# Performance work log

Measured on AMD Instinct MI355X. Metric: run time of the kernel, lower is better.

## Reference

```python
import jax, jax.numpy as jnp
import numpy as np

B, T, D, N, K, H = 2, 2048, 2048, 16, 8, 128
WINDOW = 1024
SOFT_CAP = 50.0
Q_SCALE = H ** -0.5  # query_pre_attn_scalar
ROPE_BASE = 10000
ROPE_SCALE = 1.0
K_MASK = -2.3819763e38


def apply_rope(x, positions, base_frequency=ROPE_BASE, scale_factor=ROPE_SCALE):
    # x: [B, T, n, H], positions: [B, T]
    head_dim = x.shape[-1]
    fraction = 2.0 * jnp.arange(head_dim // 2, dtype=jnp.float32) / head_dim
    timescale = base_frequency ** fraction  # [H/2]
    sin_inp = positions[..., None].astype(jnp.float32) / timescale  # [B,T,H/2]
    sin_inp = sin_inp[..., None, :] / scale_factor  # [B,T,1,H/2]
    sin, cos = jnp.sin(sin_inp), jnp.cos(sin_inp)
    x1, x2 = jnp.split(x, 2, axis=-1)
    out = jnp.concatenate([x1 * cos - x2 * sin, x2 * cos + x1 * sin], axis=-1)
    return out.astype(x.dtype)


def rms_norm(x, scale, eps=1e-6):
    var = jnp.mean(jnp.square(x.astype(jnp.float32)), axis=-1, keepdims=True)
    normed = x * jax.lax.rsqrt(var + eps)
    return (normed * (1.0 + scale)).astype(x.dtype)


def setup_inputs() -> dict:
    key = jax.random.key(0)
    ks = jax.random.split(key, 4)
    x = jax.random.normal(ks[0], (B, T, D), jnp.float32)
    segment_pos = jnp.tile(jnp.arange(T, dtype=jnp.int32)[None, :], (B, 1))
    attn_mask = jnp.tril(jnp.ones((T, T), dtype=bool))[None].repeat(B, axis=0)
    w_q = jax.random.normal(ks[1], (N, D, H), jnp.float32) * (D ** -0.5)
    w_kv = jax.random.normal(ks[2], (2, K, D, H), jnp.float32) * (D ** -0.5)
    w_o = jax.random.normal(ks[3], (N, H, D), jnp.float32) * ((N * H) ** -0.5)
    q_norm_scale = jnp.zeros((H,), jnp.float32)
    k_norm_scale = jnp.zeros((H,), jnp.float32)
    return dict(x=x, w_q=w_q, w_kv=w_kv, w_o=w_o,
                q_norm_scale=q_norm_scale, k_norm_scale=k_norm_scale,
                segment_pos=segment_pos, attn_mask=attn_mask)


def reference(x, w_q, w_kv, w_o, q_norm_scale, k_norm_scale, segment_pos, attn_mask):
    # projections
    q = jnp.einsum('BTD,NDH->BTNH', x, w_q)              # [B,T,N,H]
    kv = jnp.einsum('BSD,CKDH->CBSKH', x, w_kv)          # [2,B,S,K,H]
    k, v = kv[0], kv[1]
    # QK RMSNorm
    q = rms_norm(q, q_norm_scale)
    k = rms_norm(k, k_norm_scale)
    # RoPE + query scaling
    q = apply_rope(q, segment_pos) * Q_SCALE
    k = apply_rope(k, segment_pos)
    # GQA logits
    G = N // K
    qg = q.reshape(B, T, K, G, H)
    logits = jnp.einsum('BTKGH,BSKH->BTKGS', qg, k).reshape(B, T, N, T)
    # soft cap
    logits = jnp.tanh(logits / SOFT_CAP) * SOFT_CAP
    # sliding-window mask combined with causal attn_mask
    pos_q = segment_pos[:, :, None]
    pos_k = segment_pos[:, None, :]
    sliding = (pos_k > pos_q - WINDOW) & (pos_k < pos_q + WINDOW)
    mask = attn_mask & sliding                           # [B,T,S]
    padded = jnp.where(mask[:, :, None, :], logits, K_MASK)
    probs = jax.nn.softmax(padded, axis=-1).astype(k.dtype)
    # GQA weighted values
    enc = jnp.einsum('BTKGS,BSKH->BTKGH', probs.reshape(B, T, K, G, T), v)
    enc = enc.reshape(B, T, N, H)
    # split/concat of navigator vs scribe heads is an identity on output
    return jnp.einsum('BTNH,NHD->BTD', enc, w_o)
```

## Files before the change

kernel.cpp:

```cpp
#include <hip/hip_runtime.h>
#include <hip/hip_bf16.h>
#include <stdint.h>

typedef __attribute__((ext_vector_type(8))) short short8;
typedef __attribute__((ext_vector_type(4))) float f32x4;

#define B_ 2
#define T_ 2048
#define D_ 2048
#define N_ 16
#define KH_ 8
#define H_ 128
#define WINDOW_ 1024

__device__ __forceinline__ uint16_t f2bf(float f) {
  union { float f; uint32_t u; } a; a.f = f;
  uint32_t u = a.u;
  return (uint16_t)((u + 0x7FFFu + ((u >> 16) & 1u)) >> 16);
}
__device__ __forceinline__ float bf2f(uint16_t u) {
  union { uint32_t u; float f; } a; a.u = (uint32_t)u << 16;
  return a.f;
}

__device__ __forceinline__ void gl_lds16(const void* g, void* l) {
  __builtin_amdgcn_global_load_lds((const __attribute__((address_space(1))) void*)g,
                                   (__attribute__((address_space(3))) void*)l, 16, 0, 0);
}

__global__ __launch_bounds__(256) void k_f2b4(const float* __restrict__ src,
                                              uint16_t* __restrict__ dst, long n) {
  long i = ((long)blockIdx.x * 256 + threadIdx.x) * 4;
  if (i >= n) return;
  float4 v = *(const float4*)(src + i);
  uint64_t p = (uint64_t)f2bf(v.x) | ((uint64_t)f2bf(v.y) << 16) |
               ((uint64_t)f2bf(v.z) << 32) | ((uint64_t)f2bf(v.w) << 48);
  *(uint64_t*)(dst + i) = p;
}

__global__ __launch_bounds__(256)
void k_prep_qkv(const float* __restrict__ w_q, const float* __restrict__ w_kv,
                uint16_t* __restrict__ wq_t, uint16_t* __restrict__ wkv_t) {
  __shared__ float tile[32][33];
  int z = blockIdx.z;
  const float* s;
  uint16_t* d;
  if (z < 16) {
    s = w_q + (long)z * D_ * H_;
    d = wq_t + (long)z * H_ * D_;
  } else if (z < 24) {
    s = w_kv + (long)(z - 16) * D_ * H_;
    d = wkv_t + (long)(z - 16) * H_ * D_;
  } else {
    s = w_kv + (long)KH_ * D_ * H_ + (long)(z - 24) * D_ * H_;
    d = wkv_t + (long)1024 * 2048 + (long)(z - 24) * H_ * D_;
  }
  int c0 = blockIdx.x * 32, r0 = blockIdx.y * 32;
  int x = threadIdx.x, y = threadIdx.y;
#pragma unroll
  for (int j = 0; j < 4; ++j)
    tile[y + j * 8][x] = s[(long)(r0 + y + j * 8) * H_ + (c0 + x)];
  __syncthreads();
#pragma unroll
  for (int j = 0; j < 4; ++j)
    d[(long)(c0 + y + j * 8) * D_ + (r0 + x)] = f2bf(tile[x][y + j * 8]);
}

__global__ __launch_bounds__(256)
void k_transpose_f2b(const float* __restrict__ src, uint16_t* __restrict__ dst,
                     int R, int C, int nb1, long sbs1, long sbs2, long dbs,
                     long src_off, int srs) {
  __shared__ float tile[32][33];
  int z = blockIdx.z;
  int b1 = z % nb1, b2 = z / nb1;
  const float* s = src + src_off + (long)b1 * sbs1 + (long)b2 * sbs2;
  uint16_t* d = dst + (long)z * dbs;
  int c0 = blockIdx.x * 32, r0 = blockIdx.y * 32;
  int x = threadIdx.x, y = threadIdx.y;
#pragma unroll
  for (int j = 0; j < 4; ++j)
    tile[y + j * 8][x] = s[(long)(r0 + y + j * 8) * srs + (c0 + x)];
  __syncthreads();
#pragma unroll
  for (int j = 0; j < 4; ++j)
    d[(long)(c0 + y + j * 8) * R + (r0 + x)] = f2bf(tile[x][y + j * 8]);
}

__global__ __launch_bounds__(256)
void k_transpose_v(const uint16_t* __restrict__ kvg, uint16_t* __restrict__ vbt) {
  __shared__ uint16_t tile[32][33];
  int z = blockIdx.z;
  int kh = z % KH_, b = z / KH_;
  const uint16_t* s = kvg + (long)b * T_ * 2048 + 1024 + kh * H_;
  uint16_t* d = vbt + (long)z * H_ * T_;
  int h0 = blockIdx.x * 32, s0 = blockIdx.y * 32;
  int x = threadIdx.x, y = threadIdx.y;
#pragma unroll
  for (int j = 0; j < 4; ++j)
    tile[y + j * 8][x] = s[(long)(s0 + y + j * 8) * 2048 + (h0 + x)];
  __syncthreads();
#pragma unroll
  for (int j = 0; j < 4; ++j) {
    int h = h0 + y + j * 8;
    int si = s0 + x;
    int ss = (si & ~63) | ((((si >> 3) & 7) ^ (h & 7)) << 3) | (si & 7);
    d[(long)h * T_ + ss] = tile[x][y + j * 8];
  }
}

__global__ __launch_bounds__(512, 2)
void k_gemm8(const uint16_t* __restrict__ A, const uint16_t* __restrict__ Bt,
             uint16_t* __restrict__ C0, uint16_t* __restrict__ C1, int nbx, int splitc) {
  __shared__ __align__(16) uint16_t Ls[2][2][2][128 * 64];
  int tid = threadIdx.x, lane = tid & 63, w = tid >> 6;
  int wm = w >> 2, wn = w & 3;
  int fr = lane & 15, fgrp = lane >> 4;
  int bid = blockIdx.x;
  int k2 = bid >> 3;
  long by = (bid & 7) * 2 + k2 / nbx;
  long bx = k2 % nbx;
  long row0 = by * 256, col0 = bx * 256;

  int trow = tid >> 3;
  int kse = (((tid & 7) * 16) ^ ((trow & 7) << 4)) >> 1;
  const uint16_t* aS[2] = { A + (row0 + trow) * 2048 + kse,
                            A + (row0 + 128 + trow) * 2048 + kse };
  const uint16_t* bS[2] = { Bt + (col0 + trow) * 2048 + kse,
                            Bt + (col0 + 128 + trow) * 2048 + kse };
  char* ldsbase = (char*)Ls + w * 1024;

  int kx[2] = { (fgrp * 16) ^ ((fr & 7) << 4), (64 + fgrp * 16) ^ ((fr & 7) << 4) };
  int aoffb = (wm * 64 + fr) * 128;
  int boffb = (wn * 32 + fr) * 128;
  const char* LA = (const char*)Ls;
  const char* LB = LA + 65536;

  f32x4 acc[2][2][4][2];
#pragma unroll
  for (int qm = 0; qm < 2; ++qm)
#pragma unroll
    for (int qn = 0; qn < 2; ++qn)
#pragma unroll
      for (int m = 0; m < 4; ++m)
#pragma unroll
        for (int n = 0; n < 2; ++n) acc[qm][qn][m][n] = (f32x4){0.f, 0.f, 0.f, 0.f};

  short8 RA[4][2];
  short8 RB[2][2][2];

#define STG(MAT, SLOT, HALF, KT) do {                                      \
    const uint16_t* _g = (MAT ? bS[HALF] : aS[HALF]) + (KT) * 64;          \
    char* _l = ldsbase + (MAT) * 65536 + (SLOT) * 32768 + (HALF) * 16384;  \
    gl_lds16(_g, _l);                                                      \
    gl_lds16(_g + 64 * 2048, _l + 8192);                                   \
  } while (0)

#define RDA(SLOT, QM) do {                                                             \
    _Pragma("unroll") for (int m = 0; m < 4; ++m) {                                    \
      RA[m][0] = *(const short8*)(LA + (SLOT)*32768 + (QM)*16384 + aoffb + m*2048 + kx[0]); \
      RA[m][1] = *(const short8*)(LA + (SLOT)*32768 + (QM)*16384 + aoffb + m*2048 + kx[1]); } \
  } while (0)

#define RDB(SLOT, QN) do {                                                             \
    _Pragma("unroll") for (int n = 0; n < 2; ++n) {                                    \
      RB[QN][n][0] = *(const short8*)(LB + (SLOT)*32768 + (QN)*16384 + boffb + n*2048 + kx[0]); \
      RB[QN][n][1] = *(const short8*)(LB + (SLOT)*32768 + (QN)*16384 + boffb + n*2048 + kx[1]); } \
  } while (0)

#define PHX(RDSTMT, STGSTMT, QM, QN, VM) do {                                         \
    RDSTMT;                                                                           \
    STGSTMT;                                                                          \
    __builtin_amdgcn_s_barrier();                                                     \
    asm volatile("s_waitcnt lgkmcnt(0)" ::: "memory");                                \
    __builtin_amdgcn_sched_barrier(0);                                                \
    __builtin_amdgcn_s_setprio(1);                                                    \
    _Pragma("unroll") for (int m = 0; m < 4; ++m)                                     \
      _Pragma("unroll") for (int n = 0; n < 2; ++n) {                                 \
        acc[QM][QN][m][n] = __builtin_amdgcn_mfma_f32_16x16x32_bf16(RA[m][0], RB[QN][n][0], acc[QM][QN][m][n], 0, 0, 0); \
        acc[QM][QN][m][n] = __builtin_amdgcn_mfma_f32_16x16x32_bf16(RA[m][1], RB[QN][n][1], acc[QM][QN][m][n], 0, 0, 0); } \
    __builtin_amdgcn_s_setprio(0);                                                    \
    if (VM) { asm volatile("s_waitcnt vmcnt(8)" ::: "memory");                        \
              __builtin_amdgcn_sched_barrier(0); }                                    \
    __builtin_amdgcn_s_barrier();                                                     \
    __builtin_amdgcn_sched_barrier(0);                                                \
  } while (0)

  STG(0, 0, 0, 0); STG(1, 0, 0, 0); STG(1, 0, 1, 0); STG(0, 0, 1, 0);
  STG(0, 1, 0, 1); STG(1, 1, 0, 1); STG(1, 1, 1, 1); STG(0, 1, 1, 1);
  asm volatile("s_waitcnt vmcnt(8)" ::: "memory");
  __builtin_amdgcn_sched_barrier(0);
  __builtin_amdgcn_s_barrier();

#pragma unroll 1
  for (int it = 0; it < 16; ++it) {
    int t2 = (2 * it + 2) & 31, t3 = (2 * it + 3) & 31;
    PHX({ RDA(0, 0); RDB(0, 0); }, {}, 0, 0, 0);
    PHX({ RDB(0, 1); }, { STG(0, 0, 0, t2); STG(1, 0, 0, t2); }, 0, 1, 0);
    PHX({ RDA(0, 1); }, { STG(1, 0, 1, t2); }, 1, 1, 0);
    PHX({}, { STG(0, 0, 1, t2); }, 1, 0, 1);
    PHX({ RDA(1, 0); RDB(1, 0); }, {}, 0, 0, 0);
    PHX({ RDB(1, 1); }, { STG(0, 1, 0, t3); STG(1, 1, 0, t3); }, 0, 1, 0);
    PHX({ RDA(1, 1); }, { STG(1, 1, 1, t3); }, 1, 1, 0);
    PHX({}, { STG(0, 1, 1, t3); }, 1, 0, 1);
  }
#undef PHX
#undef RDA
#undef RDB
#undef STG

  int og = fgrp * 4;
  bool hic = (col0 >= splitc);
  uint16_t* Cb = hic ? C1 : C0;
  long cb = col0 - (hic ? splitc : 0);
#pragma unroll
  for (int qm = 0; qm < 2; ++qm)
#pragma unroll
    for (int qn = 0; qn < 2; ++qn)
#pragma unroll
      for (int m = 0; m < 4; ++m)
#pragma unroll
        for (int n = 0; n < 2; ++n) {
          long r = row0 + qm * 128 + wm * 64 + m * 16 + og;
          long c = cb + qn * 128 + wn * 32 + n * 16 + fr;
          uint16_t* cp = Cb + r * 2048 + c;
#pragma unroll
          for (int i = 0; i < 4; ++i) cp[(long)i * 2048] = f2bf(acc[qm][qn][m][n][i]);
        }
}

__global__ __launch_bounds__(512, 2)
void k_gemm8n(const uint16_t* __restrict__ A, const uint16_t* __restrict__ Bt,
              float* __restrict__ C, int nbx) {
  __shared__ __align__(16) uint16_t LsA[2][2][128 * 64];
  __shared__ __align__(16) uint16_t LsB[2][128 * 64];
  int tid = threadIdx.x, lane = tid & 63, w = tid >> 6;
  int wm = w >> 2, wn = w & 3;
  int fr = lane & 15, fgrp = lane >> 4;
  int bid = blockIdx.x;
  int k2 = bid >> 3;
  long by = (bid & 7) * 2 + k2 / nbx;
  long bx = k2 % nbx;
  long row0 = by * 256, col0 = bx * 128;

  int trow = tid >> 3;
  int kse = (((tid & 7) * 16) ^ ((trow & 7) << 4)) >> 1;
  const uint16_t* aS[2] = { A + (row0 + trow) * 2048 + kse,
                            A + (row0 + 128 + trow) * 2048 + kse };
  const uint16_t* bS = Bt + (col0 + trow) * 2048 + kse;
  char* ldsA_w = (char*)LsA + w * 1024;
  char* ldsB_w = (char*)LsB + w * 1024;

  int kx[2] = { (fgrp * 16) ^ ((fr & 7) << 4), (64 + fgrp * 16) ^ ((fr & 7) << 4) };
  int aoffb = (wm * 64 + fr) * 128;
  int boffb = (wn * 32 + fr) * 128;
  const char* LA = (const char*)LsA;
  const char* LB = (const char*)LsB;

  f32x4 acc[2][4][2];
#pragma unroll
  for (int qm = 0; qm < 2; ++qm)
#pragma unroll
    for (int m = 0; m < 4; ++m)
#pragma unroll
      for (int n = 0; n < 2; ++n) acc[qm][m][n] = (f32x4){0.f, 0.f, 0.f, 0.f};

#define STGA(SLOT, HALF, KT) do {                                \
    const uint16_t* _g = aS[HALF] + (KT) * 64;                   \
    char* _l = ldsA_w + (SLOT) * 32768 + (HALF) * 16384;         \
    gl_lds16(_g, _l);                                            \
    gl_lds16(_g + 64 * 2048, _l + 8192);                         \
  } while (0)
#define STGB(SLOT, KT) do {                                      \
    const uint16_t* _g = bS + (KT) * 64;                         \
    char* _l = ldsB_w + (SLOT) * 16384;                          \
    gl_lds16(_g, _l);                                            \
    gl_lds16(_g + 64 * 2048, _l + 8192);                         \
  } while (0)

#define PHN(SLOT, QM, STMT, VM) do {                                                  \
    short8 _a[4][2], _b[2][2];                                                        \
    _Pragma("unroll") for (int m = 0; m < 4; ++m) {                                   \
      _a[m][0] = *(const short8*)(LA + (SLOT)*32768 + (QM)*16384 + aoffb + m*2048 + kx[0]); \
      _a[m][1] = *(const short8*)(LA + (SLOT)*32768 + (QM)*16384 + aoffb + m*2048 + kx[1]); } \
    _Pragma("unroll") for (int n = 0; n < 2; ++n) {                                   \
      _b[n][0] = *(const short8*)(LB + (SLOT)*16384 + boffb + n*2048 + kx[0]);        \
      _b[n][1] = *(const short8*)(LB + (SLOT)*16384 + boffb + n*2048 + kx[1]); }      \
    STMT;                                                                             \
    __builtin_amdgcn_s_barrier();                                                     \
    asm volatile("s_waitcnt lgkmcnt(0)" ::: "memory");                                \
    __builtin_amdgcn_sched_barrier(0);                                                \
    __builtin_amdgcn_s_setprio(1);                                                    \
    _Pragma("unroll") for (int m = 0; m < 4; ++m)                                     \
      _Pragma("unroll") for (int n = 0; n < 2; ++n) {                                 \
        acc[QM][m][n] = __builtin_amdgcn_mfma_f32_16x16x32_bf16(_a[m][0], _b[n][0], acc[QM][m][n], 0, 0, 0); \
        acc[QM][m][n] = __builtin_amdgcn_mfma_f32_16x16x32_bf16(_a[m][1], _b[n][1], acc[QM][m][n], 0, 0, 0); } \
    __builtin_amdgcn_s_setprio(0);                                                    \
    if (VM) { asm volatile("s_waitcnt vmcnt(2)" ::: "memory");                        \
              __builtin_amdgcn_sched_barrier(0); }                                    \
    __builtin_amdgcn_s_barrier();                                                     \
    __builtin_amdgcn_sched_barrier(0);                                                \
  } while (0)

  STGA(0, 0, 0); STGA(0, 1, 0); STGB(0, 0); STGA(1, 0, 1);
  asm volatile("s_waitcnt vmcnt(2)" ::: "memory");
  __builtin_amdgcn_sched_barrier(0);
  __builtin_amdgcn_s_barrier();

#pragma unroll 1
  for (int it = 0; it < 16; ++it) {
    int t1 = 2 * it + 1, t2 = (2 * it + 2) & 31, t3 = (2 * it + 3) & 31;
    PHN(0, 0, { STGA(1, 1, t1); STGB(1, t1); }, 0);
    PHN(0, 1, STGA(0, 0, t2), 1);
    PHN(1, 0, { STGA(0, 1, t2); STGB(0, t2); }, 0);
    PHN(1, 1, STGA(1, 0, t3), 1);
  }
#undef PHN
#undef STGA
#undef STGB

  int og = fgrp * 4;
#pragma unroll
  for (int qm = 0; qm < 2; ++qm)
#pragma unroll
    for (int m = 0; m < 4; ++m)
#pragma unroll
      for (int n = 0; n < 2; ++n) {
        long r = row0 + qm * 128 + wm * 64 + m * 16 + og;
        long c = col0 + wn * 32 + n * 16 + fr;
        float* cp = C + r * 2048 + c;
#pragma unroll
        for (int i = 0; i < 4; ++i) cp[(long)i * 2048] = acc[qm][m][n][i];
      }
}

__global__ __launch_bounds__(256)
void k_qpost(const uint16_t* __restrict__ qg, const float* __restrict__ qs,
             uint16_t* __restrict__ qb) {
  int gw = blockIdx.x * 4 + (threadIdx.x >> 6);
  int lane = threadIdx.x & 63;
  int bt = gw / N_;
  int t = bt % T_;
  const uint16_t* src = qg + (long)gw * H_;
  float x1 = bf2f(src[lane]), x2 = bf2f(src[lane + 64]);
  float ssq = x1 * x1 + x2 * x2;
#pragma unroll
  for (int off = 1; off < 64; off <<= 1) ssq += __shfl_xor(ssq, off);
  float inv = rsqrtf(ssq * (1.0f / 128.0f) + 1e-6f);
  float n1 = x1 * inv * (1.0f + qs[lane]);
  float n2 = x2 * inv * (1.0f + qs[lane + 64]);
  float ts = powf(10000.0f, (float)lane * (2.0f / 128.0f));
  float ang = (float)t / ts;
  float sn, cs;
  sincosf(ang, &sn, &cs);
  const float QSC = 0.08838834764831845f;
  uint16_t* dp = qb + (long)gw * H_;
  dp[lane] = f2bf((n1 * cs - n2 * sn) * QSC);
  dp[lane + 64] = f2bf((n2 * cs + n1 * sn) * QSC);
}

__global__ __launch_bounds__(256)
void k_kpost(const uint16_t* __restrict__ kvg, const float* __restrict__ ks,
             uint16_t* __restrict__ kb) {
  int gw = blockIdx.x * 4 + (threadIdx.x >> 6);
  int lane = threadIdx.x & 63;
  int kh = gw % KH_;
  int bt = gw / KH_;
  int t = bt % T_, b = bt / T_;
  const uint16_t* src = kvg + (long)bt * (KH_ * H_ * 2) + kh * H_;
  float x1 = bf2f(src[lane]), x2 = bf2f(src[lane + 64]);
  float ssq = x1 * x1 + x2 * x2;
#pragma unroll
  for (int off = 1; off < 64; off <<= 1) ssq += __shfl_xor(ssq, off);
  float inv = rsqrtf(ssq * (1.0f / 128.0f) + 1e-6f);
  float n1 = x1 * inv * (1.0f + ks[lane]);
  float n2 = x2 * inv * (1.0f + ks[lane + 64]);
  float ts = powf(10000.0f, (float)lane * (2.0f / 128.0f));
  float ang = (float)t / ts;
  float sn, cs;
  sincosf(ang, &sn, &cs);
  int sw = (t & 7) << 3;
  uint16_t* dp = kb + ((long)(b * KH_ + kh) * T_ + t) * H_;
  dp[lane ^ sw] = f2bf(n1 * cs - n2 * sn);
  dp[(lane + 64) ^ sw] = f2bf(n2 * cs + n1 * sn);
}

__global__ __launch_bounds__(256, 2)
void k_attn(const uint16_t* __restrict__ qb, const uint16_t* __restrict__ kb,
            const uint16_t* __restrict__ vbt, uint16_t* __restrict__ enc) {
  __shared__ uint16_t Ks[2][64 * 128];
  __shared__ uint16_t Vs[2][128 * 64];
  __shared__ uint16_t Pl[4][16 * 64];
  int tid = threadIdx.x, lane = tid & 63, w = tid >> 6;
  int nt = T_ / 64;
  int blk = blockIdx.x;
  int tq = nt - 1 - (blk >> 5);
  int bn = blk & 31;
  int n = bn % N_, b = bn / N_;
  int kh = n >> 1;
  int t0 = tq * 64;
  int tw = t0 + w * 16;
  int fr = lane & 15, fgrp = lane >> 4, fk = fgrp * 8;
  int sw3 = fr & 7;

  const uint16_t* qrow = qb + ((long)(b * T_ + tw + fr) * N_ + n) * H_;
  short8 aq[4];
#pragma unroll
  for (int kk = 0; kk < 4; ++kk) aq[kk] = *(const short8*)(qrow + kk * 32 + fk);

  float lrow[4];
  f32x4 o[8];
#pragma unroll
  for (int i = 0; i < 4; ++i) lrow[i] = 0.0f;
#pragma unroll
  for (int hf = 0; hf < 8; ++hf) o[hf] = (f32x4){0.f, 0.f, 0.f, 0.f};

  int s_begin = t0 - (WINDOW_ - 1);
  if (s_begin < 0) s_begin = 0;
  s_begin &= ~63;
  int s_endex = t0 + 64;
  int nloc = (s_endex - s_begin) >> 6;

  const uint16_t* kbase = kb + (long)(b * KH_ + kh) * T_ * H_;
  const uint16_t* vbase = vbt + (long)(b * KH_ + kh) * H_ * T_;
  int krow_st = tid >> 4, kcol_st = (tid & 15) * 8;
  int vrow_st = tid >> 3, vcol_st = (tid & 7) * 8;
  uint16_t* Pw = Pl[w];

#define STAGEKV(BUF, S0) do {                                                        \
    char* _lk = (char*)Ks + (BUF) * 16384 + w * 1024;                                \
    char* _lv = (char*)Vs + (BUF) * 16384 + w * 1024;                                \
    _Pragma("unroll") for (int j = 0; j < 4; ++j) {                                  \
      gl_lds16(kbase + (long)((S0) + j * 16 + krow_st) * H_ + kcol_st, _lk + j * 4096); \
      gl_lds16(vbase + (long)(j * 32 + vrow_st) * T_ + (S0) + vcol_st, _lv + j * 4096); \
    }                                                                                \
  } while (0)

  STAGEKV(0, s_begin);
  __syncthreads();

  for (int it = 0; it < nloc; ++it) {
    int s0 = s_begin + (it << 6);
    int cur = it & 1;
    if (it + 1 < nloc) STAGEKV(cur ^ 1, s0 + 64);

    if (!(s0 > tw + 15 || s0 + 63 < tw - (WINDOW_ - 1))) {
      const uint16_t* Kc = (const uint16_t*)Ks + cur * 8192;
      const uint16_t* Vc = (const uint16_t*)Vs + cur * 8192;

      f32x4 sc[4];
#pragma unroll
      for (int kc = 0; kc < 4; ++kc) {
        f32x4 a = (f32x4){0.f, 0.f, 0.f, 0.f};
        const uint16_t* kr = Kc + (kc * 16 + fr) * 128;
#pragma unroll
        for (int kk = 0; kk < 4; ++kk) {
          short8 bk = *(const short8*)(kr + ((((kk << 2) | fgrp) ^ sw3) << 3));
          a = __builtin_amdgcn_mfma_f32_16x16x32_bf16(aq[kk], bk, a, 0, 0, 0);
        }
        sc[kc] = a;
      }

      bool full = (s0 + 63 <= tw) && (s0 >= tw + 16 - WINDOW_);
#define SMBODY(FULL)                                                              \
      _Pragma("unroll") for (int i = 0; i < 4; ++i) {                             \
        int r = fgrp * 4 + i;                                                     \
        int rsw = (r & 7) << 3;                                                   \
        int trowq = tw + r;                                                       \
        float ps = 0.f;                                                           \
        _Pragma("unroll") for (int kc = 0; kc < 4; ++kc) {                        \
          float v = sc[kc][i];                                                    \
          float u = v * v * 4.0e-4f;                                              \
          float t50 = v * fmaf(u, fmaf(u, fmaf(u, -0.053968254f, 0.13333334f),    \
                                       -0.33333334f), 1.0f);                      \
          float p = __expf(t50 - 20.0f);                                          \
          if (!(FULL)) {                                                          \
            int s = s0 + kc * 16 + fr;                                            \
            bool ok = (s <= trowq) && (s > trowq - WINDOW_);                      \
            p = ok ? p : 0.0f;                                                    \
          }                                                                       \
          ps += p;                                                                \
          *(__hip_bfloat16*)(Pw + r * 64 + ((kc * 16 + fr) ^ rsw)) =              \
              __float2bfloat16(p);                                                \
        }                                                                         \
        lrow[i] += ps;                                                            \
      }
      if (full) { SMBODY(true) } else { SMBODY(false) }
#undef SMBODY

      short8 pa0 = *(const short8*)(Pw + fr * 64 + ((fgrp ^ sw3) << 3));
      short8 pa1 = *(const short8*)(Pw + fr * 64 + (((4 | fgrp) ^ sw3) << 3));
#pragma unroll
      for (int hf = 0; hf < 8; ++hf) {
        const uint16_t* vr = Vc + (hf * 16 + fr) * 64;
        short8 bv0 = *(const short8*)(vr + ((fgrp ^ sw3) << 3));
        short8 bv1 = *(const short8*)(vr + (((4 | fgrp) ^ sw3) << 3));
        o[hf] = __builtin_amdgcn_mfma_f32_16x16x32_bf16(pa0, bv0, o[hf], 0, 0, 0);
        o[hf] = __builtin_amdgcn_mfma_f32_16x16x32_bf16(pa1, bv1, o[hf], 0, 0, 0);
      }
    }
    __syncthreads();
  }
#undef STAGEKV

#pragma unroll
  for (int i = 0; i < 4; ++i) {
#pragma unroll
    for (int off = 1; off < 16; off <<= 1) lrow[i] += __shfl_xor(lrow[i], off);
    lrow[i] = 1.0f / lrow[i];
  }
#pragma unroll
  for (int hf = 0; hf < 8; ++hf)
#pragma unroll
    for (int i = 0; i < 4; ++i) {
      int t = tw + fgrp * 4 + i;
      float val = o[hf][i] * lrow[i];
      enc[((long)(b * T_ + t) * N_ + n) * H_ + hf * 16 + fr] = f2bf(val);
    }
}

extern "C" void kernel_launch(void* const* d_in, const int* in_sizes, int n_in,
                              void* d_out, int out_size, void* d_ws, size_t ws_size,
                              hipStream_t stream) {
  const float* x = (const float*)d_in[0];
  const float* w_q = (const float*)d_in[1];
  const float* w_kv = (const float*)d_in[2];
  const float* w_o = (const float*)d_in[3];
  const float* qns = (const float*)d_in[4];
  const float* kns = (const float*)d_in[5];
  float* out = (float*)d_out;

  uint16_t* ws = (uint16_t*)d_ws;
  uint16_t* xb    = ws;
  uint16_t* wq_t  = xb    + 8388608;
  uint16_t* wkv_t = wq_t  + 4194304;
  uint16_t* wo_t  = wkv_t + 4194304;
  uint16_t* qb    = wo_t  + 4194304;
  uint16_t* kb    = qb    + 8388608;
  uint16_t* vbt   = kb    + 4194304;
  uint16_t* enc   = vbt   + 4194304;
  uint16_t* qg_b  = enc   + 8388608;
  uint16_t* kvg_b = qg_b  + 8388608;
  if (ws_size < (size_t)125829120) return;

  dim3 tb(32, 8);
  k_f2b4<<<8192, 256, 0, stream>>>(x, xb, 8388608);
  k_prep_qkv<<<dim3(4, 64, 32), tb, 0, stream>>>(w_q, w_kv, wq_t, wkv_t);
  k_transpose_f2b<<<dim3(64, 64, 1), tb, 0, stream>>>(w_o, wo_t, 2048, 2048, 1,
      0, 0, 0, 0, 2048);
  k_gemm8<<<256, 512, 0, stream>>>(xb, wq_t, qg_b, kvg_b, 16, 2048);
  k_qpost<<<(B_ * T_ * N_) / 4, 256, 0, stream>>>(qg_b, qns, qb);
  k_kpost<<<(B_ * T_ * KH_) / 4, 256, 0, stream>>>(kvg_b, kns, kb);
  k_transpose_v<<<dim3(4, 64, 16), tb, 0, stream>>>(kvg_b, vbt);
  k_attn<<<B_ * N_ * (T_ / 64), 256, 0, stream>>>(qb, kb, vbt, enc);
  k_gemm8n<<<256, 512, 0, stream>>>(enc, wo_t, out, 16);
}
```

Measured before the change: 228.1 us.

## Stage K/V through registers with single LDS buffer and raise occupancy

```diff
diff --git a/kernel.cpp b/kernel.cpp
--- a/kernel.cpp
+++ b/kernel.cpp
@@ -4,6 +4,7 @@
 
 typedef __attribute__((ext_vector_type(8))) short short8;
 typedef __attribute__((ext_vector_type(4))) float f32x4;
+typedef __attribute__((ext_vector_type(4))) int i32x4;
 
 #define B_ 2
 #define T_ 2048
@@ -384,11 +385,11 @@
   dp[(lane + 64) ^ sw] = f2bf(n2 * cs + n1 * sn);
 }
 
-__global__ __launch_bounds__(256, 2)
+__global__ __launch_bounds__(256, 4)
 void k_attn(const uint16_t* __restrict__ qb, const uint16_t* __restrict__ kb,
             const uint16_t* __restrict__ vbt, uint16_t* __restrict__ enc) {
-  __shared__ uint16_t Ks[2][64 * 128];
-  __shared__ uint16_t Vs[2][128 * 64];
+  __shared__ uint16_t Ks[64 * 128];
+  __shared__ uint16_t Vs[128 * 64];
   __shared__ uint16_t Pl[4][16 * 64];
   int tid = threadIdx.x, lane = tid & 63, w = tid >> 6;
   int nt = T_ / 64;
@@ -425,33 +426,38 @@
   int krow_st = tid >> 4, kcol_st = (tid & 15) * 8;
   int vrow_st = tid >> 3, vcol_st = (tid & 7) * 8;
   uint16_t* Pw = Pl[w];
-
-#define STAGEKV(BUF, S0) do {                                                        \
-    char* _lk = (char*)Ks + (BUF) * 16384 + w * 1024;                                \
-    char* _lv = (char*)Vs + (BUF) * 16384 + w * 1024;                                \
+  char* wK = (char*)Ks + w * 1024 + lane * 16;
+  char* wV = (char*)Vs + w * 1024 + lane * 16;
+
+  i32x4 pk[4], pv[4];
+
+#define LOADKV(S0) do {                                                              \
     _Pragma("unroll") for (int j = 0; j < 4; ++j) {                                  \
-      gl_lds16(kbase + (long)((S0) + j * 16 + krow_st) * H_ + kcol_st, _lk + j * 4096); \
-      gl_lds16(vbase + (long)(j * 32 + vrow_st) * T_ + (S0) + vcol_st, _lv + j * 4096); \
+      pk[j] = *(const i32x4*)(kbase + (long)((S0) + j * 16 + krow_st) * H_ + kcol_st); \
+      pv[j] = *(const i32x4*)(vbase + (long)(j * 32 + vrow_st) * T_ + (S0) + vcol_st); \
     }                                                                                \
   } while (0)
-
-  STAGEKV(0, s_begin);
+#define WRITEKV() do {                                                               \
+    _Pragma("unroll") for (int j = 0; j < 4; ++j) {                                  \
+      *(i32x4*)(wK + j * 4096) = pk[j];                                              \
+      *(i32x4*)(wV + j * 4096) = pv[j];                                              \
+    }                                                                                \
+  } while (0)
+
+  LOADKV(s_begin);
+  WRITEKV();
   __syncthreads();
 
   for (int it = 0; it < nloc; ++it) {
     int s0 = s_begin + (it << 6);
-    int cur = it & 1;
-    if (it + 1 < nloc) STAGEKV(cur ^ 1, s0 + 64);
+    if (it + 1 < nloc) LOADKV(s0 + 64);
 
     if (!(s0 > tw + 15 || s0 + 63 < tw - (WINDOW_ - 1))) {
-      const uint16_t* Kc = (const uint16_t*)Ks + cur * 8192;
-      const uint16_t* Vc = (const uint16_t*)Vs + cur * 8192;
-
       f32x4 sc[4];
 #pragma unroll
       for (int kc = 0; kc < 4; ++kc) {
         f32x4 a = (f32x4){0.f, 0.f, 0.f, 0.f};
-        const uint16_t* kr = Kc + (kc * 16 + fr) * 128;
+        const uint16_t* kr = Ks + (kc * 16 + fr) * 128;
 #pragma unroll
         for (int kk = 0; kk < 4; ++kk) {
           short8 bk = *(const short8*)(kr + ((((kk << 2) | fgrp) ^ sw3) << 3));
@@ -491,7 +497,7 @@
       short8 pa1 = *(const short8*)(Pw + fr * 64 + (((4 | fgrp) ^ sw3) << 3));
 #pragma unroll
       for (int hf = 0; hf < 8; ++hf) {
-        const uint16_t* vr = Vc + (hf * 16 + fr) * 64;
+        const uint16_t* vr = Vs + (hf * 16 + fr) * 64;
         short8 bv0 = *(const short8*)(vr + ((fgrp ^ sw3) << 3));
         short8 bv1 = *(const short8*)(vr + (((4 | fgrp) ^ sw3) << 3));
         o[hf] = __builtin_amdgcn_mfma_f32_16x16x32_bf16(pa0, bv0, o[hf], 0, 0, 0);
@@ -499,8 +505,13 @@
       }
     }
     __syncthreads();
+    if (it + 1 < nloc) {
+      WRITEKV();
+      __syncthreads();
+    }
   }
-#undef STAGEKV
+#undef LOADKV
+#undef WRITEKV
 
 #pragma unroll
   for (int i = 0; i < 4; ++i) {
```

Measured after the change: 314.7 us. 1.38x slower.
